# Kernel tuning notes

Hardware: AMD Instinct MI355X
Metric: run time of the kernel (lower is better)

Reference implementation:

```python
import jax, jax.numpy as jnp
import numpy as np

DIM = 256
FOCAL_LEVELS = (3, 5, 7)  # odd kernels so padding=k//2 preserves length
B, L = 8, 16384


def _dwconv(x, k):
    # x: [B, C, L], k: [C, 1, K] depthwise kernel (groups=C)
    pad = k.shape[-1] // 2
    return jax.lax.conv_general_dilated(
        x, k, window_strides=(1,), padding=[(pad, pad)],
        dimension_numbers=('NCH', 'OIH', 'NCH'),
        feature_group_count=x.shape[1])


def setup_inputs() -> dict:
    key = jax.random.key(0)
    ks = jax.random.split(key, 13)
    C = DIM
    G = len(FOCAL_LEVELS) + 1
    s = jnp.float32(0.02)
    inp = {
        'x': jax.random.normal(ks[0], (B, C, L), jnp.float32),
        'q_w': jax.random.normal(ks[1], (C, C), jnp.float32) * s,
        'q_b': jax.random.normal(ks[2], (C,), jnp.float32) * s,
        'v_w': jax.random.normal(ks[3], (C, C), jnp.float32) * s,
        'v_b': jax.random.normal(ks[4], (C,), jnp.float32) * s,
        'g_w': jax.random.normal(ks[5], (G, C), jnp.float32) * s,
        'g_b': jax.random.normal(ks[6], (G,), jnp.float32) * s,
        'f0_w': jax.random.normal(ks[7], (C, 1, FOCAL_LEVELS[0]), jnp.float32) * s,
        'f1_w': jax.random.normal(ks[8], (C, 1, FOCAL_LEVELS[1]), jnp.float32) * s,
        'f2_w': jax.random.normal(ks[9], (C, 1, FOCAL_LEVELS[2]), jnp.float32) * s,
        'mix_w': jax.random.normal(ks[10], (C, C), jnp.float32) * s,
        'mix_b': jax.random.normal(ks[11], (C,), jnp.float32) * s,
    }
    return inp


def reference(x, q_w, q_b, v_w, v_b, g_w, g_b, f0_w, f1_w, f2_w, mix_w, mix_b):
    gelu = lambda t: jax.nn.gelu(t, approximate=False)  # torch GELU default = exact erf
    # Linear weights are [out, in]; contract over channel axis of [B, C, L]
    focus = jnp.einsum('bcl,ec->bel', x, v_w) + v_b[None, :, None]   # [B, C, L]
    gates = jnp.einsum('bcl,gc->bgl', x, g_w) + g_b[None, :, None]   # [B, 4, L]
    query = jnp.einsum('bcl,ec->bel', x, q_w) + q_b[None, :, None]   # [B, C, L]

    kernels = (f0_w, f1_w, f2_w)  # fixed small set: loop over levels is fine
    focus = gelu(_dwconv(focus, kernels[0]))
    acc = focus * gates[:, 0:1, :]
    for i in range(1, len(kernels)):
        focus = gelu(_dwconv(focus, kernels[i]))
        acc = acc + focus * gates[:, i:i + 1, :]

    # global focus: mean over length, GELU, broadcast across length via gate
    global_focus = gelu(jnp.mean(focus, axis=2, keepdims=True))      # [B, C, 1]
    acc = acc + global_focus * gates[:, len(kernels):len(kernels) + 1, :]

    # mix_depth: 1x1 conv == pointwise linear over channels
    acc = jnp.einsum('bcl,oc->bol', acc, mix_w) + mix_b[None, :, None]
    mask = jax.nn.softmax(acc, axis=-1)  # softmax over length
    out = jax.nn.sigmoid(query) * mask
    return (out, mask)
```

## Files before the change

kernel.cpp:

```cpp
#include <hip/hip_runtime.h>

#define LLEN 16384
#define PAD 258

typedef short bf16x8 __attribute__((ext_vector_type(8)));
typedef float f32x4 __attribute__((ext_vector_type(4)));

__device__ __forceinline__ short f2bf(float f) {
  union { float f; unsigned u; } v; v.f = f;
  unsigned r = (v.u + 0x7FFFu + ((v.u >> 16) & 1u)) >> 16;
  return (short)r;
}
__device__ __forceinline__ float bf2f(short s) {
  union { unsigned u; float f; } v;
  v.u = ((unsigned)(unsigned short)s) << 16;
  return v.f;
}
__device__ __forceinline__ float geluf(float x) {
  return 0.5f * x * (1.0f + erff(x * 0.70710678118654752f));
}
__device__ __forceinline__ float waveRedSum(float v) {
  #pragma unroll
  for (int o = 32; o > 0; o >>= 1) v += __shfl_xor(v, o, 64);
  return v;
}
__device__ __forceinline__ float waveRedMax(float v) {
  #pragma unroll
  for (int o = 32; o > 0; o >>= 1) v = fmaxf(v, __shfl_xor(v, o, 64));
  return v;
}

__global__ __launch_bounds__(256) void k0_convert(
    const float* __restrict__ qw, const float* __restrict__ vw,
    const float* __restrict__ gw, const float* __restrict__ mw,
    short* __restrict__ qwb, short* __restrict__ vwb,
    short* __restrict__ gwb, short* __restrict__ mwb,
    float* __restrict__ rowsum) {
  int idx = blockIdx.x * 256 + threadIdx.x;
  qwb[idx] = f2bf(qw[idx]);
  vwb[idx] = f2bf(vw[idx]);
  mwb[idx] = f2bf(mw[idx]);
  if (idx < 4096) {
    int r = idx >> 8, c = idx & 255;
    gwb[idx] = (r < 4) ? f2bf(gw[r * 256 + c]) : (short)0;
  }
  if (idx < 2048) rowsum[idx] = 0.f;
}

__device__ __forceinline__ void gemm64(const short* __restrict__ wmat,
                                       const short xs[64][PAD], int lane,
                                       f32x4 acc[4][4]) {
  int r = lane & 15, h = lane >> 4;
  #pragma unroll
  for (int k0 = 0; k0 < 256; k0 += 32) {
    bf16x8 bfr[4];
    #pragma unroll
    for (int lf = 0; lf < 4; ++lf)
      bfr[lf] = *(const bf16x8*)&xs[lf * 16 + r][k0 + 8 * h];
    #pragma unroll
    for (int ef = 0; ef < 4; ++ef) {
      bf16x8 afr = *(const bf16x8*)(wmat + (ef * 16 + r) * 256 + k0 + 8 * h);
      #pragma unroll
      for (int lf = 0; lf < 4; ++lf)
        acc[ef][lf] = __builtin_amdgcn_mfma_f32_16x16x32_bf16(afr, bfr[lf],
                                                              acc[ef][lf], 0, 0, 0);
    }
  }
}

__global__ __launch_bounds__(256) void k1_qvg(
    const float* __restrict__ x, const short* __restrict__ vwb,
    const short* __restrict__ qwb, const short* __restrict__ gwb,
    const float* __restrict__ v_b, const float* __restrict__ q_b,
    const float* __restrict__ g_b, short* __restrict__ focus0,
    short* __restrict__ qzS, float* __restrict__ gates) {
  int b = blockIdx.x >> 8, lt = blockIdx.x & 255;
  int l0 = lt << 6;
  __shared__ short xs[64][PAD];
  int t = threadIdx.x;
  {
    int l = t & 63, cg = t >> 6;
    const float* xb = x + ((size_t)b << 22) + l0 + l;
    #pragma unroll 4
    for (int rep = 0; rep < 32; ++rep) {
      int c = rep * 8 + cg * 2;
      float a0 = xb[(size_t)c << 14];
      float a1 = xb[((size_t)c + 1) << 14];
      unsigned pk = (unsigned)(unsigned short)f2bf(a0) |
                    ((unsigned)(unsigned short)f2bf(a1) << 16);
      *(unsigned*)&xs[l][c] = pk;
    }
  }
  __syncthreads();
  int lane = t & 63, wave = t >> 6;
  int r = lane & 15, h = lane >> 4;
  int e0 = wave << 6;
  f32x4 acc[4][4];

  #pragma unroll
  for (int ef = 0; ef < 4; ++ef)
    #pragma unroll
    for (int lf = 0; lf < 4; ++lf)
      acc[ef][lf] = (f32x4){0.f, 0.f, 0.f, 0.f};
  gemm64(vwb + e0 * 256, xs, lane, acc);
  #pragma unroll
  for (int ef = 0; ef < 4; ++ef) {
    #pragma unroll
    for (int i = 0; i < 4; ++i) {
      int e = e0 + ef * 16 + 4 * h + i;
      float bias = v_b[e];
      size_t rowoff = (size_t)((b << 8) | e) << 14;
      #pragma unroll
      for (int lf = 0; lf < 4; ++lf) {
        int li = l0 + lf * 16 + r;
        focus0[rowoff + li] = f2bf(acc[ef][lf][i] + bias);
      }
    }
  }

  #pragma unroll
  for (int ef = 0; ef < 4; ++ef)
    #pragma unroll
    for (int lf = 0; lf < 4; ++lf)
      acc[ef][lf] = (f32x4){0.f, 0.f, 0.f, 0.f};
  gemm64(qwb + e0 * 256, xs, lane, acc);
  #pragma unroll
  for (int ef = 0; ef < 4; ++ef) {
    #pragma unroll
    for (int i = 0; i < 4; ++i) {
      int e = e0 + ef * 16 + 4 * h + i;
      float bias = q_b[e];
      size_t rowoff = ((size_t)((b << 8) | e) << 15) + 16384;
      #pragma unroll
      for (int lf = 0; lf < 4; ++lf) {
        int li = l0 + lf * 16 + r;
        qzS[rowoff + li] = f2bf(acc[ef][lf][i] + bias);
      }
    }
  }

  if (wave == 0) {
    f32x4 gacc[4];
    #pragma unroll
    for (int lf = 0; lf < 4; ++lf) gacc[lf] = (f32x4){0.f, 0.f, 0.f, 0.f};
    #pragma unroll
    for (int k0 = 0; k0 < 256; k0 += 32) {
      bf16x8 afr = *(const bf16x8*)(gwb + r * 256 + k0 + 8 * h);
      #pragma unroll
      for (int lf = 0; lf < 4; ++lf) {
        bf16x8 bfr = *(const bf16x8*)&xs[lf * 16 + r][k0 + 8 * h];
        gacc[lf] = __builtin_amdgcn_mfma_f32_16x16x32_bf16(afr, bfr, gacc[lf], 0, 0, 0);
      }
    }
    if (h == 0) {
      #pragma unroll
      for (int i = 0; i < 4; ++i) {
        float gb = g_b[i];
        size_t goff = (size_t)((b << 2) | i) << 14;
        #pragma unroll
        for (int lf = 0; lf < 4; ++lf)
          gates[goff + l0 + lf * 16 + r] = gacc[lf][i] + gb;
      }
    }
  }
}

__global__ __launch_bounds__(256) void k2_conv(
    const short* __restrict__ focus0, const float* __restrict__ gates,
    const float* __restrict__ f0_w, const float* __restrict__ f1_w,
    const float* __restrict__ f2_w, short* __restrict__ acc3S,
    float* __restrict__ rowsum) {
  int bx = blockIdx.x;
  int b = bx >> 12, c = (bx >> 4) & 255, lt = bx & 15;
  int l0 = lt << 10;
  __shared__ float s0[1036], s1[1034], s2[1030];
  __shared__ float rs[4];
  int t = threadIdx.x;
  const short* fp = focus0 + ((size_t)((b << 8) | c) << 14);
  for (int i = t; i < 1036; i += 256) {
    int gl = l0 - 6 + i;
    s0[i] = (gl >= 0 && gl < LLEN) ? bf2f(fp[gl]) : 0.f;
  }
  float w0[3], w1[5], w2[7];
  #pragma unroll
  for (int j = 0; j < 3; ++j) w0[j] = f0_w[c * 3 + j];
  #pragma unroll
  for (int j = 0; j < 5; ++j) w1[j] = f1_w[c * 5 + j];
  #pragma unroll
  for (int j = 0; j < 7; ++j) w2[j] = f2_w[c * 7 + j];
  __syncthreads();
  for (int i = t; i < 1034; i += 256) {
    int gl = l0 - 5 + i;
    float z = w0[0] * s0[i] + w0[1] * s0[i + 1] + w0[2] * s0[i + 2];
    s1[i] = (gl >= 0 && gl < LLEN) ? geluf(z) : 0.f;
  }
  __syncthreads();
  for (int i = t; i < 1030; i += 256) {
    int gl = l0 - 3 + i;
    float z = w1[0] * s1[i] + w1[1] * s1[i + 1] + w1[2] * s1[i + 2] +
              w1[3] * s1[i + 3] + w1[4] * s1[i + 4];
    s2[i] = (gl >= 0 && gl < LLEN) ? geluf(z) : 0.f;
  }
  __syncthreads();
  const float* gp = gates + ((size_t)(b << 2) << 14);
  short* op = acc3S + ((size_t)((b << 8) | c) << 15);
  float lsum = 0.f;
  #pragma unroll
  for (int ii = 0; ii < 2; ++ii) {
    int i = 2 * t + 512 * ii;
    float z0 = w2[0] * s2[i] + w2[1] * s2[i + 1] + w2[2] * s2[i + 2] +
               w2[3] * s2[i + 3] + w2[4] * s2[i + 4] + w2[5] * s2[i + 5] +
               w2[6] * s2[i + 6];
    float z1 = w2[0] * s2[i + 1] + w2[1] * s2[i + 2] + w2[2] * s2[i + 3] +
               w2[3] * s2[i + 4] + w2[4] * s2[i + 5] + w2[5] * s2[i + 6] +
               w2[6] * s2[i + 7];
    float f30 = geluf(z0), f31 = geluf(z1);
    lsum += f30 + f31;
    int l = l0 + i;
    float a0 = s1[i + 5] * gp[l] + s2[i + 3] * gp[LLEN + l] + f30 * gp[2 * LLEN + l];
    float a1 = s1[i + 6] * gp[l + 1] + s2[i + 4] * gp[LLEN + l + 1] +
               f31 * gp[2 * LLEN + l + 1];
    unsigned pk = (unsigned)(unsigned short)f2bf(a0) |
                  ((unsigned)(unsigned short)f2bf(a1) << 16);
    *(unsigned*)&op[l] = pk;
  }
  float wsv = waveRedSum(lsum);
  if ((t & 63) == 0) rs[t >> 6] = wsv;
  __syncthreads();
  if (t == 0) atomicAdd(&rowsum[(b << 8) | c], rs[0] + rs[1] + rs[2] + rs[3]);
}

__global__ __launch_bounds__(256) void k3_gf(const float* __restrict__ rowsum,
                                             float* __restrict__ gf) {
  int i = blockIdx.x * 256 + threadIdx.x;
  gf[i] = geluf(rowsum[i] * (1.0f / 16384.0f));
}

__global__ __launch_bounds__(256) void k4_mix(
    short* maskS, const float* __restrict__ gates, const float* __restrict__ gf,
    const short* __restrict__ mwb, const float* __restrict__ mix_b) {
  int b = blockIdx.x >> 8, lt = blockIdx.x & 255;
  int l0 = lt << 6;
  __shared__ short xs[64][PAD];
  int t = threadIdx.x;
  {
    int l = t & 63, cg = t >> 6;
    float g3 = gates[((size_t)((b << 2) | 3) << 14) + l0 + l];
    const float* gfp = gf + (b << 8);
    const short* ap = maskS + ((size_t)(b << 8) << 15) + l0 + l;
    #pragma unroll 4
    for (int rep = 0; rep < 32; ++rep) {
      int c = rep * 8 + cg * 2;
      float a0 = bf2f(ap[(size_t)c << 15]) + gfp[c] * g3;
      float a1 = bf2f(ap[((size_t)c + 1) << 15]) + gfp[c + 1] * g3;
      unsigned pk = (unsigned)(unsigned short)f2bf(a0) |
                    ((unsigned)(unsigned short)f2bf(a1) << 16);
      *(unsigned*)&xs[l][c] = pk;
    }
  }
  __syncthreads();
  int lane = t & 63, wave = t >> 6;
  int r = lane & 15, h = lane >> 4;
  int e0 = wave << 6;
  f32x4 acc[4][4];
  #pragma unroll
  for (int ef = 0; ef < 4; ++ef)
    #pragma unroll
    for (int lf = 0; lf < 4; ++lf)
      acc[ef][lf] = (f32x4){0.f, 0.f, 0.f, 0.f};
  gemm64(mwb + e0 * 256, xs, lane, acc);
  #pragma unroll
  for (int ef = 0; ef < 4; ++ef) {
    #pragma unroll
    for (int i = 0; i < 4; ++i) {
      int o = e0 + ef * 16 + 4 * h + i;
      float bias = mix_b[o];
      size_t rowoff = ((size_t)((b << 8) | o) << 15) + 16384;
      #pragma unroll
      for (int lf = 0; lf < 4; ++lf) {
        int li = l0 + lf * 16 + r;
        maskS[rowoff + li] = f2bf(acc[ef][lf][i] + bias);
      }
    }
  }
}

__global__ __launch_bounds__(512) void k5_softmax(
    const short* __restrict__ maskS, const short* __restrict__ outS,
    float* __restrict__ maskF, float* __restrict__ outF) {
  int row = blockIdx.x;
  int t = threadIdx.x;
  const short* mrow = maskS + ((size_t)row << 15) + 16384;
  const short* qrow = outS + ((size_t)row << 15) + 16384;
  float* mw = maskF + ((size_t)row << 14);
  float* ow = outF + ((size_t)row << 14);
  int lane = t & 63, wave = t >> 6;
  bf16x8 qv[4];
  float f[32];
  float lm = -3.0e38f;
  #pragma unroll
  for (int i = 0; i < 4; ++i) {
    bf16x8 mv = *(const bf16x8*)&mrow[i * 4096 + t * 8];
    qv[i] = *(const bf16x8*)&qrow[i * 4096 + t * 8];
    #pragma unroll
    for (int j = 0; j < 8; ++j) {
      float vf = bf2f(mv[j]);
      f[i * 8 + j] = vf;
      lm = fmaxf(lm, vf);
    }
  }
  __shared__ float redm[8], reds[8];
  float wm = waveRedMax(lm);
  if (lane == 0) redm[wave] = wm;
  __syncthreads();
  float M = redm[0];
  #pragma unroll
  for (int w = 1; w < 8; ++w) M = fmaxf(M, redm[w]);
  float ls = 0.f;
  #pragma unroll
  for (int k = 0; k < 32; ++k) {
    f[k] = expf(f[k] - M);
    ls += f[k];
  }
  float wsum = waveRedSum(ls);
  if (lane == 0) reds[wave] = wsum;
  __syncthreads();
  float S = reds[0];
  #pragma unroll
  for (int w = 1; w < 8; ++w) S += reds[w];
  float inv = 1.0f / S;
  #pragma unroll
  for (int i = 0; i < 4; ++i) {
    float mk[8], oo[8];
    #pragma unroll
    for (int j = 0; j < 8; ++j) {
      mk[j] = f[i * 8 + j] * inv;
      float sig = 1.0f / (1.0f + expf(-bf2f(qv[i][j])));
      oo[j] = sig * mk[j];
    }
    float* mp = &mw[i * 4096 + t * 8];
    float* op = &ow[i * 4096 + t * 8];
    *(float4*)mp = (float4){mk[0], mk[1], mk[2], mk[3]};
    *(float4*)(mp + 4) = (float4){mk[4], mk[5], mk[6], mk[7]};
    *(float4*)op = (float4){oo[0], oo[1], oo[2], oo[3]};
    *(float4*)(op + 4) = (float4){oo[4], oo[5], oo[6], oo[7]};
  }
}

extern "C" void kernel_launch(void* const* d_in, const int* in_sizes, int n_in,
                              void* d_out, int out_size, void* d_ws, size_t ws_size,
                              hipStream_t stream) {
  const float* x     = (const float*)d_in[0];
  const float* q_w   = (const float*)d_in[1];
  const float* q_b   = (const float*)d_in[2];
  const float* v_w   = (const float*)d_in[3];
  const float* v_b   = (const float*)d_in[4];
  const float* g_w   = (const float*)d_in[5];
  const float* g_b   = (const float*)d_in[6];
  const float* f0_w  = (const float*)d_in[7];
  const float* f1_w  = (const float*)d_in[8];
  const float* f2_w  = (const float*)d_in[9];
  const float* mix_w = (const float*)d_in[10];
  const float* mix_b = (const float*)d_in[11];

  float* outbuf  = (float*)d_out;
  float* maskbuf = outbuf + (size_t)8 * 256 * 16384;
  short* outS  = (short*)outbuf;
  short* maskS = (short*)maskbuf;

  char* ws = (char*)d_ws;
  short* vwb    = (short*)(ws + 0);
  short* qwb    = (short*)(ws + 131072);
  short* mwb    = (short*)(ws + 262144);
  short* gwb    = (short*)(ws + 393216);
  float* rowsum = (float*)(ws + 401408);
  float* gf     = (float*)(ws + 409600);
  float* gates  = (float*)(ws + 417792);
  short* focus0 = (short*)(ws + 2514944);

  k0_convert<<<dim3(256), dim3(256), 0, stream>>>(q_w, v_w, g_w, mix_w,
                                                  qwb, vwb, gwb, mwb, rowsum);
  k1_qvg<<<dim3(2048), dim3(256), 0, stream>>>(x, vwb, qwb, gwb, v_b, q_b, g_b,
                                               focus0, outS, gates);
  k2_conv<<<dim3(32768), dim3(256), 0, stream>>>(focus0, gates, f0_w, f1_w, f2_w,
                                                 maskS, rowsum);
  k3_gf<<<dim3(8), dim3(256), 0, stream>>>(rowsum, gf);
  k4_mix<<<dim3(2048), dim3(256), 0, stream>>>(maskS, gates, gf, mwb, mix_b);
  k5_softmax<<<dim3(2048), dim3(512), 0, stream>>>(maskS, outS, maskbuf, outbuf);
}
```

Baseline: 363.9 us.

## Swap MFMA operands for vectorized epilogue stores and widen staging loads

```diff
diff --git a/kernel.cpp b/kernel.cpp
--- a/kernel.cpp
+++ b/kernel.cpp
@@ -6,11 +6,11 @@
 typedef short bf16x8 __attribute__((ext_vector_type(8)));
 typedef float f32x4 __attribute__((ext_vector_type(4)));
 
-__device__ __forceinline__ short f2bf(float f) {
+__device__ __forceinline__ unsigned bfbits(float f) {
   union { float f; unsigned u; } v; v.f = f;
-  unsigned r = (v.u + 0x7FFFu + ((v.u >> 16) & 1u)) >> 16;
-  return (short)r;
-}
+  return (v.u + 0x7FFFu + ((v.u >> 16) & 1u)) >> 16;
+}
+__device__ __forceinline__ short f2bf(float f) { return (short)bfbits(f); }
 __device__ __forceinline__ float bf2f(short s) {
   union { unsigned u; float f; } v;
   v.u = ((unsigned)(unsigned short)s) << 16;
@@ -53,19 +53,26 @@
   int r = lane & 15, h = lane >> 4;
   #pragma unroll
   for (int k0 = 0; k0 < 256; k0 += 32) {
-    bf16x8 bfr[4];
-    #pragma unroll
-    for (int lf = 0; lf < 4; ++lf)
-      bfr[lf] = *(const bf16x8*)&xs[lf * 16 + r][k0 + 8 * h];
+    bf16x8 xfr[4];
+    #pragma unroll
+    for (int lf = 0; lf < 4; ++lf)
+      xfr[lf] = *(const bf16x8*)&xs[lf * 16 + r][k0 + 8 * h];
     #pragma unroll
     for (int ef = 0; ef < 4; ++ef) {
-      bf16x8 afr = *(const bf16x8*)(wmat + (ef * 16 + r) * 256 + k0 + 8 * h);
+      bf16x8 wfr = *(const bf16x8*)(wmat + (ef * 16 + r) * 256 + k0 + 8 * h);
       #pragma unroll
       for (int lf = 0; lf < 4; ++lf)
-        acc[ef][lf] = __builtin_amdgcn_mfma_f32_16x16x32_bf16(afr, bfr[lf],
+        acc[ef][lf] = __builtin_amdgcn_mfma_f32_16x16x32_bf16(xfr[lf], wfr,
                                                               acc[ef][lf], 0, 0, 0);
     }
   }
+}
+
+__device__ __forceinline__ void store_bf4(short* p, f32x4 a, float bias) {
+  uint2 pk;
+  pk.x = bfbits(a[0] + bias) | (bfbits(a[1] + bias) << 16);
+  pk.y = bfbits(a[2] + bias) | (bfbits(a[3] + bias) << 16);
+  *(uint2*)p = pk;
 }
 
 __global__ __launch_bounds__(256) void k1_qvg(
@@ -79,16 +86,15 @@
   __shared__ short xs[64][PAD];
   int t = threadIdx.x;
   {
-    int l = t & 63, cg = t >> 6;
-    const float* xb = x + ((size_t)b << 22) + l0 + l;
+    int l2 = (t & 31) * 2, cg = t >> 5;
+    const float* xb = x + ((size_t)b << 22) + l0 + l2;
     #pragma unroll 4
-    for (int rep = 0; rep < 32; ++rep) {
-      int c = rep * 8 + cg * 2;
-      float a0 = xb[(size_t)c << 14];
-      float a1 = xb[((size_t)c + 1) << 14];
-      unsigned pk = (unsigned)(unsigned short)f2bf(a0) |
-                    ((unsigned)(unsigned short)f2bf(a1) << 16);
-      *(unsigned*)&xs[l][c] = pk;
+    for (int rep = 0; rep < 16; ++rep) {
+      int c = rep * 16 + cg * 2;
+      float2 a = *(const float2*)&xb[(size_t)c << 14];
+      float2 bb = *(const float2*)&xb[((size_t)c + 1) << 14];
+      *(unsigned*)&xs[l2][c] = bfbits(a.x) | (bfbits(bb.x) << 16);
+      *(unsigned*)&xs[l2 + 1][c] = bfbits(a.y) | (bfbits(bb.y) << 16);
     }
   }
   __syncthreads();
@@ -105,61 +111,51 @@
   gemm64(vwb + e0 * 256, xs, lane, acc);
   #pragma unroll
   for (int ef = 0; ef < 4; ++ef) {
-    #pragma unroll
-    for (int i = 0; i < 4; ++i) {
-      int e = e0 + ef * 16 + 4 * h + i;
-      float bias = v_b[e];
-      size_t rowoff = (size_t)((b << 8) | e) << 14;
+    int e = e0 + ef * 16 + r;
+    float bias = v_b[e];
+    short* rowp = focus0 + ((size_t)((b << 8) | e) << 14) + l0 + 4 * h;
+    #pragma unroll
+    for (int lf = 0; lf < 4; ++lf)
+      store_bf4(rowp + lf * 16, acc[ef][lf], bias);
+  }
+
+  #pragma unroll
+  for (int ef = 0; ef < 4; ++ef)
+    #pragma unroll
+    for (int lf = 0; lf < 4; ++lf)
+      acc[ef][lf] = (f32x4){0.f, 0.f, 0.f, 0.f};
+  gemm64(qwb + e0 * 256, xs, lane, acc);
+  #pragma unroll
+  for (int ef = 0; ef < 4; ++ef) {
+    int e = e0 + ef * 16 + r;
+    float bias = q_b[e];
+    short* rowp = qzS + (((size_t)((b << 8) | e) << 15) + 16384) + l0 + 4 * h;
+    #pragma unroll
+    for (int lf = 0; lf < 4; ++lf)
+      store_bf4(rowp + lf * 16, acc[ef][lf], bias);
+  }
+
+  if (wave == 0) {
+    f32x4 gacc[4];
+    #pragma unroll
+    for (int lf = 0; lf < 4; ++lf) gacc[lf] = (f32x4){0.f, 0.f, 0.f, 0.f};
+    #pragma unroll
+    for (int k0 = 0; k0 < 256; k0 += 32) {
+      bf16x8 wfr = *(const bf16x8*)(gwb + r * 256 + k0 + 8 * h);
       #pragma unroll
       for (int lf = 0; lf < 4; ++lf) {
-        int li = l0 + lf * 16 + r;
-        focus0[rowoff + li] = f2bf(acc[ef][lf][i] + bias);
+        bf16x8 xfr = *(const bf16x8*)&xs[lf * 16 + r][k0 + 8 * h];
+        gacc[lf] = __builtin_amdgcn_mfma_f32_16x16x32_bf16(xfr, wfr, gacc[lf], 0, 0, 0);
       }
     }
-  }
-
-  #pragma unroll
-  for (int ef = 0; ef < 4; ++ef)
-    #pragma unroll
-    for (int lf = 0; lf < 4; ++lf)
-      acc[ef][lf] = (f32x4){0.f, 0.f, 0.f, 0.f};
-  gemm64(qwb + e0 * 256, xs, lane, acc);
-  #pragma unroll
-  for (int ef = 0; ef < 4; ++ef) {
-    #pragma unroll
-    for (int i = 0; i < 4; ++i) {
-      int e = e0 + ef * 16 + 4 * h + i;
-      float bias = q_b[e];
-      size_t rowoff = ((size_t)((b << 8) | e) << 15) + 16384;
+    if (r < 4) {
+      float gb = g_b[r];
+      float* gp = gates + (((size_t)((b << 2) | r)) << 14) + l0 + 4 * h;
       #pragma unroll
       for (int lf = 0; lf < 4; ++lf) {
-        int li = l0 + lf * 16 + r;
-        qzS[rowoff + li] = f2bf(acc[ef][lf][i] + bias);
-      }
-    }
-  }
-
-  if (wave == 0) {
-    f32x4 gacc[4];
-    #pragma unroll
-    for (int lf = 0; lf < 4; ++lf) gacc[lf] = (f32x4){0.f, 0.f, 0.f, 0.f};
-    #pragma unroll
-    for (int k0 = 0; k0 < 256; k0 += 32) {
-      bf16x8 afr = *(const bf16x8*)(gwb + r * 256 + k0 + 8 * h);
-      #pragma unroll
-      for (int lf = 0; lf < 4; ++lf) {
-        bf16x8 bfr = *(const bf16x8*)&xs[lf * 16 + r][k0 + 8 * h];
-        gacc[lf] = __builtin_amdgcn_mfma_f32_16x16x32_bf16(afr, bfr, gacc[lf], 0, 0, 0);
-      }
-    }
-    if (h == 0) {
-      #pragma unroll
-      for (int i = 0; i < 4; ++i) {
-        float gb = g_b[i];
-        size_t goff = (size_t)((b << 2) | i) << 14;
-        #pragma unroll
-        for (int lf = 0; lf < 4; ++lf)
-          gates[goff + l0 + lf * 16 + r] = gacc[lf][i] + gb;
+        float4 o = {gacc[lf][0] + gb, gacc[lf][1] + gb,
+                    gacc[lf][2] + gb, gacc[lf][3] + gb};
+        *(float4*)(gp + lf * 16) = o;
       }
     }
   }
@@ -220,9 +216,7 @@
     float a0 = s1[i + 5] * gp[l] + s2[i + 3] * gp[LLEN + l] + f30 * gp[2 * LLEN + l];
     float a1 = s1[i + 6] * gp[l + 1] + s2[i + 4] * gp[LLEN + l + 1] +
                f31 * gp[2 * LLEN + l + 1];
-    unsigned pk = (unsigned)(unsigned short)f2bf(a0) |
-                  ((unsigned)(unsigned short)f2bf(a1) << 16);
-    *(unsigned*)&op[l] = pk;
+    *(unsigned*)&op[l] = bfbits(a0) | (bfbits(a1) << 16);
   }
   float wsv = waveRedSum(lsum);
   if ((t & 63) == 0) rs[t >> 6] = wsv;
@@ -244,18 +238,23 @@
   __shared__ short xs[64][PAD];
   int t = threadIdx.x;
   {
-    int l = t & 63, cg = t >> 6;
-    float g3 = gates[((size_t)((b << 2) | 3) << 14) + l0 + l];
+    int l2 = (t & 31) * 2, cg = t >> 5;
+    float2 g3v = *(const float2*)(gates + (((size_t)((b << 2) | 3)) << 14) + l0 + l2);
     const float* gfp = gf + (b << 8);
-    const short* ap = maskS + ((size_t)(b << 8) << 15) + l0 + l;
+    const unsigned short* ap =
+        (const unsigned short*)maskS + (((size_t)(b << 8)) << 15) + l0 + l2;
     #pragma unroll 4
-    for (int rep = 0; rep < 32; ++rep) {
-      int c = rep * 8 + cg * 2;
-      float a0 = bf2f(ap[(size_t)c << 15]) + gfp[c] * g3;
-      float a1 = bf2f(ap[((size_t)c + 1) << 15]) + gfp[c + 1] * g3;
-      unsigned pk = (unsigned)(unsigned short)f2bf(a0) |
-                    ((unsigned)(unsigned short)f2bf(a1) << 16);
-      *(unsigned*)&xs[l][c] = pk;
+    for (int rep = 0; rep < 16; ++rep) {
+      int c = rep * 16 + cg * 2;
+      unsigned av = *(const unsigned*)&ap[(size_t)c << 15];
+      unsigned bv = *(const unsigned*)&ap[((size_t)c + 1) << 15];
+      float gf0 = gfp[c], gf1 = gfp[c + 1];
+      float a0 = bf2f((short)(av & 0xFFFF)) + gf0 * g3v.x;
+      float a1 = bf2f((short)(av >> 16)) + gf0 * g3v.y;
+      float b0 = bf2f((short)(bv & 0xFFFF)) + gf1 * g3v.x;
+      float b1 = bf2f((short)(bv >> 16)) + gf1 * g3v.y;
+      *(unsigned*)&xs[l2][c] = bfbits(a0) | (bfbits(b0) << 16);
+      *(unsigned*)&xs[l2 + 1][c] = bfbits(a1) | (bfbits(b1) << 16);
     }
   }
   __syncthreads();
@@ -271,17 +270,12 @@
   gemm64(mwb + e0 * 256, xs, lane, acc);
   #pragma unroll
   for (int ef = 0; ef < 4; ++ef) {
-    #pragma unroll
-    for (int i = 0; i < 4; ++i) {
-      int o = e0 + ef * 16 + 4 * h + i;
-      float bias = mix_b[o];
-      size_t rowoff = ((size_t)((b << 8) | o) << 15) + 16384;
-      #pragma unroll
-      for (int lf = 0; lf < 4; ++lf) {
-        int li = l0 + lf * 16 + r;
-        maskS[rowoff + li] = f2bf(acc[ef][lf][i] + bias);
-      }
-    }
+    int o = e0 + ef * 16 + r;
+    float bias = mix_b[o];
+    short* rowp = maskS + (((size_t)((b << 8) | o) << 15) + 16384) + l0 + 4 * h;
+    #pragma unroll
+    for (int lf = 0; lf < 4; ++lf)
+      store_bf4(rowp + lf * 16, acc[ef][lf], bias);
   }
 }
 
```

After: 376.2 us. 3.4% more time.
